# Performance work log

Measured on AMD Instinct MI355X. Metric: run time of the kernel, lower is better.

The kernel has to match this reference:

```python
import jax, jax.numpy as jnp
import numpy as np

B, S, D = 1, 2048, 1024
L, H, NH = 256, 1024, 16  # latent_dim, hidden_dim, num_heads
HD = H // NH
EPS = 1e-6


def rmsnorm(x, g):
    return x * jax.lax.rsqrt(jnp.mean(x * x, axis=-1, keepdims=True) + EPS) * g


def setup_inputs() -> dict:
    key = jax.random.key(0)
    ks = jax.random.split(key, 16)
    def w(k, shape, fan_in):
        return jax.random.normal(k, shape, jnp.float32) / np.sqrt(fan_in)
    return {
        "x": jax.random.normal(ks[0], (B, S, D), jnp.float32),
        "g1": jnp.ones((D,), jnp.float32),
        "Wq": w(ks[1], (D, H), D), "bq": jnp.zeros((H,), jnp.float32),
        "Wdown": w(ks[2], (D, L), D), "bdown": jnp.zeros((L,), jnp.float32),
        "Wk": w(ks[3], (L, H), L), "bk": jnp.zeros((H,), jnp.float32),
        "Wv": w(ks[4], (L, H), L), "bv": jnp.zeros((H,), jnp.float32),
        "Wo": w(ks[5], (H, D), H), "bo": jnp.zeros((D,), jnp.float32),
        "g2": jnp.ones((D,), jnp.float32),
        "W1": w(ks[6], (D, 4 * D), D), "b1": jnp.zeros((4 * D,), jnp.float32),
        "W2": w(ks[7], (4 * D, D), 4 * D), "b2": jnp.zeros((D,), jnp.float32),
    }


def reference(x, g1, Wq, bq, Wdown, bdown, Wk, bk, Wv, bv, Wo, bo, g2, W1, b1, W2, b2):
    stream = x
    # RMSNorm -> MLA (low-rank latent KV attention, causal)
    h = rmsnorm(x, g1)
    q = (h @ Wq + bq).reshape(B, S, NH, HD)
    c = h @ Wdown + bdown                       # [B,S,L] compressed KV latent
    k = (c @ Wk + bk).reshape(B, S, NH, HD)
    v = (c @ Wv + bv).reshape(B, S, NH, HD)
    scores = jnp.einsum("bqhd,bkhd->bhqk", q, k) / np.sqrt(HD)
    causal = jnp.tril(jnp.ones((S, S), bool))
    scores = jnp.where(causal, scores, jnp.finfo(scores.dtype).min)
    attn = jax.nn.softmax(scores, axis=-1)
    o = jnp.einsum("bhqk,bkhd->bqhd", attn, v).reshape(B, S, H)
    stream = (o @ Wo + bo) + stream
    # RMSNorm -> FFN (D -> 4D -> D, activation on every layer incl. last)
    h = rmsnorm(stream, g2)
    h = jax.nn.silu(h @ W1 + b1)
    h = jax.nn.silu(h @ W2 + b2)
    return h + stream
```

## Files before the change

### kernel.cpp

```cpp
#include <hip/hip_runtime.h>

typedef __bf16 bf16x8 __attribute__((ext_vector_type(8)));
typedef float  f32x4  __attribute__((ext_vector_type(4)));

static __device__ __forceinline__ ushort f2bf(float f) {
    union { float f; unsigned u; } a; a.f = f;
    unsigned r = a.u + 0x7FFFu + ((a.u >> 16) & 1u);
    return (ushort)(r >> 16);
}
static __device__ __forceinline__ ushort f2bf_hw(float f) {
    __bf16 b = (__bf16)f;
    return __builtin_bit_cast(ushort, b);
}

#define TS  2048
#define TD  1024
#define TL  256
#define TH  1024
#define TNH 16
#define THD 64
#define TDF 4096
#define ATT_CE 0.18033688f

#define GLD_LDS(gp, lp) \
    __builtin_amdgcn_global_load_lds( \
        (const __attribute__((address_space(1))) unsigned int*)(gp), \
        (__attribute__((address_space(3))) unsigned int*)(lp), 16, 0, 0)

__global__ __launch_bounds__(256) void transpose_to_bf16(
    const float* __restrict__ in, ushort* __restrict__ out, int K, int N)
{
    __shared__ float tile[32][33];
    const int k0 = blockIdx.x * 32, n0 = blockIdx.y * 32;
    const int tx = threadIdx.x, ty = threadIdx.y;
#pragma unroll
    for (int i = ty; i < 32; i += 8)
        tile[i][tx] = in[(size_t)(k0 + i) * N + n0 + tx];
    __syncthreads();
#pragma unroll
    for (int i = ty; i < 32; i += 8)
        out[(size_t)(n0 + i) * K + k0 + tx] = f2bf(tile[tx][i]);
}

__global__ __launch_bounds__(256) void concat_bias_kernel(
    const float* __restrict__ a, const float* __restrict__ b,
    float* __restrict__ o, int n)
{
    const int i = blockIdx.x * 256 + threadIdx.x;
    o[i] = (i < n) ? a[i] : b[i - n];
}

__global__ __launch_bounds__(256) void rmsnorm_kernel(
    const float* __restrict__ x, const float* __restrict__ g,
    ushort* __restrict__ out, int D)
{
    const int row = blockIdx.x;
    const int tid = threadIdx.x;
    const float4 v = ((const float4*)(x + (size_t)row * D))[tid];
    float ss = v.x * v.x + v.y * v.y + v.z * v.z + v.w * v.w;
#pragma unroll
    for (int off = 32; off > 0; off >>= 1) ss += __shfl_down(ss, off);
    __shared__ float sums[4];
    if ((tid & 63) == 0) sums[tid >> 6] = ss;
    __syncthreads();
    const float tot = sums[0] + sums[1] + sums[2] + sums[3];
    const float scale = rsqrtf(tot / (float)D + 1e-6f);
    const float4 gv = ((const float4*)g)[tid];
    ushort4 o;
    o.x = f2bf(v.x * scale * gv.x);
    o.y = f2bf(v.y * scale * gv.y);
    o.z = f2bf(v.z * scale * gv.z);
    o.w = f2bf(v.w * scale * gv.w);
    *(ushort4*)(out + (size_t)row * D + tid * 4) = o;
}

template <int EPI, int BM, int BN, int BKH>
__global__ __launch_bounds__(256) void gemm_bf16_kernel(
    const ushort* __restrict__ A, const ushort* __restrict__ BT,
    const float* __restrict__ bias, const float* __restrict__ resid,
    void* __restrict__ outp, int M, int N, int K)
{
    constexpr int WM = BM / 2, WN = BN / 2;
    constexpr int MT = WM / 16, NT = WN / 16;
    constexpr int NLA = BM / 64, NLB = BN / 64;
    __shared__ alignas(16) ushort As[2][BKH][BM * 32];
    __shared__ alignas(16) ushort Bs[2][BKH][BN * 32];
    const int bm = blockIdx.y * BM, bn = blockIdx.x * BN;
    const int tid = threadIdx.x;
    const int lane = tid & 63, wave = tid >> 6;
    const int wr = (wave >> 1) * WM, wc = (wave & 1) * WN;
    const int l15 = lane & 15, l4 = lane >> 4;

    f32x4 acc[MT][NT] = {};

    const int grow = wave * 16 + (lane >> 2);
    const int gcol = (lane & 3) * 8;
    const ushort* Ag = A + (size_t)(bm + grow) * K + gcol;
    const ushort* Bg = BT + (size_t)(bn + grow) * K + gcol;

    auto stage = [&](int buf, int k0) {
#pragma unroll
        for (int h = 0; h < BKH; ++h) {
#pragma unroll
            for (int i = 0; i < NLA; ++i)
                GLD_LDS(Ag + (size_t)(i * 64) * K + k0 + h * 32,
                        &As[buf][h][(i * 64 + wave * 16) * 32]);
#pragma unroll
            for (int i = 0; i < NLB; ++i)
                GLD_LDS(Bg + (size_t)(i * 64) * K + k0 + h * 32,
                        &Bs[buf][h][(i * 64 + wave * 16) * 32]);
        }
    };

    stage(0, 0);
    asm volatile("s_waitcnt vmcnt(0)" ::: "memory");
    __syncthreads();

    const int nsteps = K / (32 * BKH);
    for (int t = 0; t < nsteps; ++t) {
        const int cur = t & 1;
        if (t + 1 < nsteps) stage(cur ^ 1, (t + 1) * 32 * BKH);

#pragma unroll
        for (int h = 0; h < BKH; ++h) {
            bf16x8 af[MT], bf[NT];
#pragma unroll
            for (int mt = 0; mt < MT; ++mt)
                af[mt] = *(const bf16x8*)&As[cur][h][(wr + mt * 16 + l15) * 32 + l4 * 8];
#pragma unroll
            for (int nt = 0; nt < NT; ++nt)
                bf[nt] = *(const bf16x8*)&Bs[cur][h][(wc + nt * 16 + l15) * 32 + l4 * 8];
#pragma unroll
            for (int mt = 0; mt < MT; ++mt)
#pragma unroll
                for (int nt = 0; nt < NT; ++nt)
                    acc[mt][nt] = __builtin_amdgcn_mfma_f32_16x16x32_bf16(
                        af[mt], bf[nt], acc[mt][nt], 0, 0, 0);
        }

        asm volatile("s_waitcnt vmcnt(0)" ::: "memory");
        __syncthreads();
    }

#pragma unroll
    for (int mt = 0; mt < MT; ++mt) {
#pragma unroll
        for (int nt = 0; nt < NT; ++nt) {
#pragma unroll
            for (int i = 0; i < 4; ++i) {
                const int row = bm + wr + mt * 16 + l4 * 4 + i;
                const int col = bn + wc + nt * 16 + l15;
                float v = acc[mt][nt][i] + bias[col];
                if constexpr (EPI == 1 || EPI == 3) v = v / (1.f + __expf(-v));
                if constexpr (EPI == 2 || EPI == 3) v += resid[(size_t)row * N + col];
                if constexpr (EPI == 0 || EPI == 1)
                    ((ushort*)outp)[(size_t)row * N + col] = f2bf(v);
                else
                    ((float*)outp)[(size_t)row * N + col] = v;
            }
        }
    }
}

__global__ __launch_bounds__(256) void mla_attn_kernel(
    const ushort* __restrict__ Q, const ushort* __restrict__ Kg,
    const ushort* __restrict__ Vg, float* __restrict__ OP, float* __restrict__ ML)
{
    constexpr int QSTR = 1024, KSTR = 2048;
    __shared__ alignas(16) ushort Ks[2][64 * 64];
    __shared__ alignas(16) ushort VTs[2][64 * 64];
    __shared__ alignas(16) ushort Ps[4][16 * 64];
    const int qb = (int)gridDim.x - 1 - (int)blockIdx.x;
    const int h = blockIdx.y;
    const int sp = blockIdx.z;
    const int tid = threadIdx.x, lane = tid & 63, wave = tid >> 6;
    const int l15 = lane & 15, l4 = lane >> 4;
    const int qrow0 = qb * 64 + wave * 16;
    const int myq = qrow0 + l15;

    const int ntile = qb + 1;
    const int half = (ntile + 1) >> 1;
    const int kt0 = sp ? half : 0;
    const int ktend = sp ? ntile : half;

    auto swzK = [](ushort* base, int row, int colbyte) -> ushort* {
        return (ushort*)((char*)base + row * 128 + (colbyte ^ ((row & 7) << 4)));
    };
    auto swzVT = [](ushort* base, int d, int colbyte) -> ushort* {
        return (ushort*)((char*)base + d * 128 + (colbyte ^ (((d >> 3) & 7) << 4)));
    };
    auto swzP = [&](int row, int colbyte) -> ushort* {
        return (ushort*)((char*)&Ps[wave][0] + row * 128 + (colbyte ^ ((row & 7) << 4)));
    };

    bf16x8 qf[2];
#pragma unroll
    for (int ks = 0; ks < 2; ++ks)
        qf[ks] = *(const bf16x8*)&Q[(size_t)(qrow0 + l15) * QSTR + h * THD + ks * 32 + l4 * 8];

    f32x4 oacc[4] = {};
    float m_run = -1e30f, l_run = 0.f;

    const int sr = tid >> 3, sc = (tid & 7) * 8;
    const ushort* kbase = Kg + (size_t)sr * KSTR + h * THD + sc;
    const ushort* vbase = Vg + (size_t)sr * KSTR + h * THD + sc;

    uint4 kr0, kr1, vr0, vr1;
    {
        const size_t off = (size_t)kt0 * 64 * KSTR;
        kr0 = *(const uint4*)(kbase + off);
        kr1 = *(const uint4*)(kbase + off + (size_t)32 * KSTR);
        vr0 = *(const uint4*)(vbase + off);
        vr1 = *(const uint4*)(vbase + off + (size_t)32 * KSTR);
    }
    {
        *(uint4*)swzK(&Ks[0][0], sr, sc * 2) = kr0;
        *(uint4*)swzK(&Ks[0][0], sr + 32, sc * 2) = kr1;
        const ushort* p0 = (const ushort*)&vr0;
        const ushort* p1 = (const ushort*)&vr1;
#pragma unroll
        for (int j = 0; j < 8; ++j) {
            *swzVT(&VTs[0][0], sc + j, sr * 2) = p0[j];
            *swzVT(&VTs[0][0], sc + j, (sr + 32) * 2) = p1[j];
        }
    }
    if (kt0 + 1 < ktend) {
        const size_t off = (size_t)(kt0 + 1) * 64 * KSTR;
        kr0 = *(const uint4*)(kbase + off);
        kr1 = *(const uint4*)(kbase + off + (size_t)32 * KSTR);
        vr0 = *(const uint4*)(vbase + off);
        vr1 = *(const uint4*)(vbase + off + (size_t)32 * KSTR);
    }

    for (int kt = kt0; kt < ktend; ++kt) {
        const int rel = kt - kt0;
        __syncthreads();
        if (kt + 1 < ktend) {
            ushort* kd = &Ks[(rel + 1) & 1][0];
            ushort* vd = &VTs[(rel + 1) & 1][0];
            *(uint4*)swzK(kd, sr, sc * 2) = kr0;
            *(uint4*)swzK(kd, sr + 32, sc * 2) = kr1;
            const ushort* p0 = (const ushort*)&vr0;
            const ushort* p1 = (const ushort*)&vr1;
#pragma unroll
            for (int j = 0; j < 8; ++j) {
                *swzVT(vd, sc + j, sr * 2) = p0[j];
                *swzVT(vd, sc + j, (sr + 32) * 2) = p1[j];
            }
            if (kt + 2 < ktend) {
                const size_t off = (size_t)(kt + 2) * 64 * KSTR;
                kr0 = *(const uint4*)(kbase + off);
                kr1 = *(const uint4*)(kbase + off + (size_t)32 * KSTR);
                vr0 = *(const uint4*)(vbase + off);
                vr1 = *(const uint4*)(vbase + off + (size_t)32 * KSTR);
            }
        }
        const ushort* kb_lds = &Ks[rel & 1][0];
        const ushort* vb_lds = &VTs[rel & 1][0];

        f32x4 s[4] = {};
        __builtin_amdgcn_s_setprio(1);
#pragma unroll
        for (int ks = 0; ks < 2; ++ks) {
#pragma unroll
            for (int nt = 0; nt < 4; ++nt) {
                const bf16x8 kf = *(const bf16x8*)swzK((ushort*)kb_lds, nt * 16 + l15, ks * 64 + l4 * 16);
                s[nt] = __builtin_amdgcn_mfma_f32_16x16x32_bf16(kf, qf[ks], s[nt], 0, 0, 0);
            }
        }
        __builtin_amdgcn_s_setprio(0);

        if (kt == qb) {
            const int kb = kt * 64;
#pragma unroll
            for (int nt = 0; nt < 4; ++nt)
#pragma unroll
                for (int i = 0; i < 4; ++i)
                    if (kb + nt * 16 + l4 * 4 + i > myq) s[nt][i] = -3.0e38f;
        }

        float mx = m_run;
#pragma unroll
        for (int nt = 0; nt < 4; ++nt)
#pragma unroll
            for (int i = 0; i < 4; ++i) mx = fmaxf(mx, s[nt][i]);
        mx = fmaxf(mx, __shfl_xor(mx, 16));
        mx = fmaxf(mx, __shfl_xor(mx, 32));
        const float alpha = exp2f((m_run - mx) * ATT_CE);
        m_run = mx;
        float ps = 0.f;
#pragma unroll
        for (int nt = 0; nt < 4; ++nt)
#pragma unroll
            for (int i = 0; i < 4; ++i) {
                const float p = exp2f((s[nt][i] - mx) * ATT_CE);
                s[nt][i] = p;
                ps += p;
            }
        ps += __shfl_xor(ps, 16);
        ps += __shfl_xor(ps, 32);
        l_run = l_run * alpha + ps;

#pragma unroll
        for (int dt = 0; dt < 4; ++dt)
#pragma unroll
            for (int i = 0; i < 4; ++i) oacc[dt][i] *= alpha;

#pragma unroll
        for (int nt = 0; nt < 4; ++nt) {
            ushort4 pk;
            pk.x = f2bf_hw(s[nt][0]); pk.y = f2bf_hw(s[nt][1]);
            pk.z = f2bf_hw(s[nt][2]); pk.w = f2bf_hw(s[nt][3]);
            *(ushort4*)swzP(l15, nt * 32 + l4 * 8) = pk;
        }

        __builtin_amdgcn_s_setprio(1);
#pragma unroll
        for (int ks = 0; ks < 2; ++ks) {
            const bf16x8 pf = *(const bf16x8*)swzP(l15, ks * 64 + l4 * 16);
#pragma unroll
            for (int dt = 0; dt < 4; ++dt) {
                const bf16x8 vf = *(const bf16x8*)swzVT((ushort*)vb_lds, dt * 16 + l15, ks * 64 + l4 * 16);
                oacc[dt] = __builtin_amdgcn_mfma_f32_16x16x32_bf16(vf, pf, oacc[dt], 0, 0, 0);
            }
        }
        __builtin_amdgcn_s_setprio(0);
    }

    float* op = OP + (size_t)sp * TS * TH;
#pragma unroll
    for (int dt = 0; dt < 4; ++dt) {
        float4 o4;
        o4.x = oacc[dt][0]; o4.y = oacc[dt][1];
        o4.z = oacc[dt][2]; o4.w = oacc[dt][3];
        *(float4*)&op[(size_t)myq * TH + h * THD + dt * 16 + l4 * 4] = o4;
    }
    if (l4 == 0) {
        float* ml = ML + (size_t)sp * TS * TNH * 2;
        ml[((size_t)myq * TNH + h) * 2 + 0] = m_run;
        ml[((size_t)myq * TNH + h) * 2 + 1] = l_run;
    }
}

__global__ __launch_bounds__(256) void attn_combine_kernel(
    const float* __restrict__ OP, const float* __restrict__ ML,
    ushort* __restrict__ O)
{
    const int idx = blockIdx.x * 256 + threadIdx.x;
    const int row = idx >> 8;
    const int h = (idx & 255) >> 4;
    const float m0 = ML[((size_t)row * TNH + h) * 2 + 0];
    const float l0 = ML[((size_t)row * TNH + h) * 2 + 1];
    const float m1 = ML[(size_t)TS * TNH * 2 + ((size_t)row * TNH + h) * 2 + 0];
    const float l1 = ML[(size_t)TS * TNH * 2 + ((size_t)row * TNH + h) * 2 + 1];
    const float M = fmaxf(m0, m1);
    const float w0 = exp2f((m0 - M) * ATT_CE);
    const float w1 = exp2f((m1 - M) * ATT_CE);
    const float inv = 1.f / (l0 * w0 + l1 * w1);
    const float4 a = ((const float4*)OP)[idx];
    const float4 b = ((const float4*)(OP + (size_t)TS * TH))[idx];
    ushort4 o;
    o.x = f2bf_hw((a.x * w0 + b.x * w1) * inv);
    o.y = f2bf_hw((a.y * w0 + b.y * w1) * inv);
    o.z = f2bf_hw((a.z * w0 + b.z * w1) * inv);
    o.w = f2bf_hw((a.w * w0 + b.w * w1) * inv);
    ((ushort4*)O)[idx] = o;
}

extern "C" void kernel_launch(void* const* d_in, const int* in_sizes, int n_in,
                              void* d_out, int out_size, void* d_ws, size_t ws_size,
                              hipStream_t stream)
{
    const float* x     = (const float*)d_in[0];
    const float* g1    = (const float*)d_in[1];
    const float* Wq    = (const float*)d_in[2];
    const float* bq    = (const float*)d_in[3];
    const float* Wdown = (const float*)d_in[4];
    const float* bdown = (const float*)d_in[5];
    const float* Wk    = (const float*)d_in[6];
    const float* bk    = (const float*)d_in[7];
    const float* Wv    = (const float*)d_in[8];
    const float* bv    = (const float*)d_in[9];
    const float* Wo    = (const float*)d_in[10];
    const float* bo    = (const float*)d_in[11];
    const float* g2    = (const float*)d_in[12];
    const float* W1    = (const float*)d_in[13];
    const float* b1    = (const float*)d_in[14];
    const float* W2    = (const float*)d_in[15];
    const float* b2    = (const float*)d_in[16];
    float* out = (float*)d_out;

    char* ws = (char*)d_ws;
    size_t off = 0;
    auto alloc = [&](size_t bytes) {
        void* p = ws + off;
        off += (bytes + 255) & ~(size_t)255;
        return p;
    };
    ushort* WqT    = (ushort*)alloc((size_t)TH * TD * 2);
    ushort* WdownT = (ushort*)alloc((size_t)TL * TD * 2);
    ushort* WkvT   = (ushort*)alloc((size_t)2 * TH * TL * 2);
    ushort* WoT    = (ushort*)alloc((size_t)TD * TH * 2);
    ushort* W1T    = (ushort*)alloc((size_t)TDF * TD * 2);
    ushort* W2T    = (ushort*)alloc((size_t)TD * TDF * 2);
    float*  bkv    = (float*)alloc((size_t)2 * TH * 4);
    ushort* hbuf   = (ushort*)alloc((size_t)TS * TD * 2);
    ushort* cbuf   = (ushort*)alloc((size_t)TS * TL * 2);
    ushort* qbuf   = (ushort*)alloc((size_t)TS * TH * 2);
    ushort* kvbuf  = (ushort*)alloc((size_t)TS * 2 * TH * 2);
    ushort* obuf   = (ushort*)alloc((size_t)TS * TH * 2);
    float*  strm   = (float*)alloc((size_t)TS * TD * 4);
    ushort* h2buf  = (ushort*)alloc((size_t)TS * TD * 2);
    ushort* ffn1   = (ushort*)alloc((size_t)TS * TDF * 2);
    float*  mlbuf  = (float*)alloc((size_t)2 * TS * TNH * 2 * 4);
    float*  opart  = (float*)ffn1;

    const dim3 tb(32, 8);
    transpose_to_bf16<<<dim3(TD / 32, TH / 32), tb, 0, stream>>>(Wq, WqT, TD, TH);
    transpose_to_bf16<<<dim3(TD / 32, TL / 32), tb, 0, stream>>>(Wdown, WdownT, TD, TL);
    transpose_to_bf16<<<dim3(TL / 32, TH / 32), tb, 0, stream>>>(Wk, WkvT, TL, TH);
    transpose_to_bf16<<<dim3(TL / 32, TH / 32), tb, 0, stream>>>(Wv, WkvT + (size_t)TH * TL, TL, TH);
    transpose_to_bf16<<<dim3(TH / 32, TD / 32), tb, 0, stream>>>(Wo, WoT, TH, TD);
    transpose_to_bf16<<<dim3(TD / 32, TDF / 32), tb, 0, stream>>>(W1, W1T, TD, TDF);
    transpose_to_bf16<<<dim3(TDF / 32, TD / 32), tb, 0, stream>>>(W2, W2T, TDF, TD);
    concat_bias_kernel<<<(2 * TH) / 256, 256, 0, stream>>>(bk, bv, bkv, TH);

    rmsnorm_kernel<<<TS, 256, 0, stream>>>(x, g1, hbuf, TD);

    gemm_bf16_kernel<0, 64, 64, 2><<<dim3(TH / 64, TS / 64), 256, 0, stream>>>(
        hbuf, WqT, bq, nullptr, qbuf, TS, TH, TD);
    gemm_bf16_kernel<0, 64, 64, 2><<<dim3(TL / 64, TS / 64), 256, 0, stream>>>(
        hbuf, WdownT, bdown, nullptr, cbuf, TS, TL, TD);
    gemm_bf16_kernel<0, 64, 64, 2><<<dim3(2 * TH / 64, TS / 64), 256, 0, stream>>>(
        cbuf, WkvT, bkv, nullptr, kvbuf, TS, 2 * TH, TL);

    mla_attn_kernel<<<dim3(TS / 64, TNH, 2), 256, 0, stream>>>(
        qbuf, kvbuf, kvbuf + TH, opart, mlbuf);
    attn_combine_kernel<<<(TS * TH / 4) / 256, 256, 0, stream>>>(
        opart, mlbuf, obuf);

    gemm_bf16_kernel<2, 64, 64, 2><<<dim3(TD / 64, TS / 64), 256, 0, stream>>>(
        obuf, WoT, bo, x, strm, TS, TD, TH);

    rmsnorm_kernel<<<TS, 256, 0, stream>>>(strm, g2, h2buf, TD);

    gemm_bf16_kernel<1, 128, 128, 1><<<dim3(TDF / 128, TS / 128), 256, 0, stream>>>(
        h2buf, W1T, b1, nullptr, ffn1, TS, TDF, TD);
    gemm_bf16_kernel<3, 64, 64, 2><<<dim3(TD / 64, TS / 64), 256, 0, stream>>>(
        ffn1, W2T, b2, strm, out, TS, TD, TDF);
}
```

Before: 216.4 us.

## Process two query groups per wave, split keys four ways, store bf16 partials

The attention kernel now covers 128 query rows per block, with each wave handling two 16-row groups. Both groups share the same K and V tiles loaded into LDS, which halves K/V staging per query row. The key range is split into four chunks instead of two, so the causal workload stays spread across the same block count. Partial outputs are written as bf16 rather than fp32 to cut combine traffic, at the cost of extra rounding. Higher register pressure from doubled accumulators, now capped by a launch bound of 4, may limit occupancy.

```diff
diff --git a/kernel.cpp b/kernel.cpp
--- a/kernel.cpp
+++ b/kernel.cpp
@@ -11,6 +11,9 @@
 static __device__ __forceinline__ ushort f2bf_hw(float f) {
     __bf16 b = (__bf16)f;
     return __builtin_bit_cast(ushort, b);
+}
+static __device__ __forceinline__ float bf2f(ushort u) {
+    return __builtin_bit_cast(float, (unsigned)u << 16);
 }
 
 #define TS  2048
@@ -21,6 +24,7 @@
 #define THD 64
 #define TDF 4096
 #define ATT_CE 0.18033688f
+#define NSPLIT 4
 
 #define GLD_LDS(gp, lp) \
     __builtin_amdgcn_global_load_lds( \
@@ -162,9 +166,9 @@
     }
 }
 
-__global__ __launch_bounds__(256) void mla_attn_kernel(
+__global__ __launch_bounds__(256, 4) void mla_attn_kernel(
     const ushort* __restrict__ Q, const ushort* __restrict__ Kg,
-    const ushort* __restrict__ Vg, float* __restrict__ OP, float* __restrict__ ML)
+    const ushort* __restrict__ Vg, ushort* __restrict__ OP, float* __restrict__ ML)
 {
     constexpr int QSTR = 1024, KSTR = 2048;
     __shared__ alignas(16) ushort Ks[2][64 * 64];
@@ -175,13 +179,14 @@
     const int sp = blockIdx.z;
     const int tid = threadIdx.x, lane = tid & 63, wave = tid >> 6;
     const int l15 = lane & 15, l4 = lane >> 4;
-    const int qrow0 = qb * 64 + wave * 16;
-    const int myq = qrow0 + l15;
-
-    const int ntile = qb + 1;
-    const int half = (ntile + 1) >> 1;
-    const int kt0 = sp ? half : 0;
-    const int ktend = sp ? ntile : half;
+    const int qrow0 = qb * 128 + wave * 32;
+    const int myqA = qrow0 + l15;
+    const int myqB = qrow0 + 16 + l15;
+
+    const int ntile = 2 * (qb + 1);
+    const int chunk = (ntile + NSPLIT - 1) / NSPLIT;
+    const int kt0 = sp * chunk;
+    const int ktend = min(ntile, kt0 + chunk);
 
     auto swzK = [](ushort* base, int row, int colbyte) -> ushort* {
         return (ushort*)((char*)base + row * 128 + (colbyte ^ ((row & 7) << 4)));
@@ -193,43 +198,45 @@
         return (ushort*)((char*)&Ps[wave][0] + row * 128 + (colbyte ^ ((row & 7) << 4)));
     };
 
-    bf16x8 qf[2];
-#pragma unroll
-    for (int ks = 0; ks < 2; ++ks)
-        qf[ks] = *(const bf16x8*)&Q[(size_t)(qrow0 + l15) * QSTR + h * THD + ks * 32 + l4 * 8];
-
-    f32x4 oacc[4] = {};
-    float m_run = -1e30f, l_run = 0.f;
+    bf16x8 qfA[2], qfB[2];
+#pragma unroll
+    for (int ks = 0; ks < 2; ++ks) {
+        qfA[ks] = *(const bf16x8*)&Q[(size_t)myqA * QSTR + h * THD + ks * 32 + l4 * 8];
+        qfB[ks] = *(const bf16x8*)&Q[(size_t)myqB * QSTR + h * THD + ks * 32 + l4 * 8];
+    }
+
+    f32x4 oaccA[4] = {}, oaccB[4] = {};
+    float mA = -1e30f, lA = 0.f, mB = -1e30f, lB = 0.f;
 
     const int sr = tid >> 3, sc = (tid & 7) * 8;
     const ushort* kbase = Kg + (size_t)sr * KSTR + h * THD + sc;
     const ushort* vbase = Vg + (size_t)sr * KSTR + h * THD + sc;
 
     uint4 kr0, kr1, vr0, vr1;
-    {
-        const size_t off = (size_t)kt0 * 64 * KSTR;
-        kr0 = *(const uint4*)(kbase + off);
-        kr1 = *(const uint4*)(kbase + off + (size_t)32 * KSTR);
-        vr0 = *(const uint4*)(vbase + off);
-        vr1 = *(const uint4*)(vbase + off + (size_t)32 * KSTR);
-    }
-    {
-        *(uint4*)swzK(&Ks[0][0], sr, sc * 2) = kr0;
-        *(uint4*)swzK(&Ks[0][0], sr + 32, sc * 2) = kr1;
-        const ushort* p0 = (const ushort*)&vr0;
-        const ushort* p1 = (const ushort*)&vr1;
-#pragma unroll
-        for (int j = 0; j < 8; ++j) {
-            *swzVT(&VTs[0][0], sc + j, sr * 2) = p0[j];
-            *swzVT(&VTs[0][0], sc + j, (sr + 32) * 2) = p1[j];
-        }
-    }
-    if (kt0 + 1 < ktend) {
-        const size_t off = (size_t)(kt0 + 1) * 64 * KSTR;
-        kr0 = *(const uint4*)(kbase + off);
-        kr1 = *(const uint4*)(kbase + off + (size_t)32 * KSTR);
-        vr0 = *(const uint4*)(vbase + off);
-        vr1 = *(const uint4*)(vbase + off + (size_t)32 * KSTR);
+    if (kt0 < ktend) {
+        {
+            const size_t off = (size_t)kt0 * 64 * KSTR;
+            kr0 = *(const uint4*)(kbase + off);
+            kr1 = *(const uint4*)(kbase + off + (size_t)32 * KSTR);
+            vr0 = *(const uint4*)(vbase + off);
+            vr1 = *(const uint4*)(vbase + off + (size_t)32 * KSTR);
+            *(uint4*)swzK(&Ks[0][0], sr, sc * 2) = kr0;
+            *(uint4*)swzK(&Ks[0][0], sr + 32, sc * 2) = kr1;
+            const ushort* p0 = (const ushort*)&vr0;
+            const ushort* p1 = (const ushort*)&vr1;
+#pragma unroll
+            for (int j = 0; j < 8; ++j) {
+                *swzVT(&VTs[0][0], sc + j, sr * 2) = p0[j];
+                *swzVT(&VTs[0][0], sc + j, (sr + 32) * 2) = p1[j];
+            }
+        }
+        if (kt0 + 1 < ktend) {
+            const size_t off = (size_t)(kt0 + 1) * 64 * KSTR;
+            kr0 = *(const uint4*)(kbase + off);
+            kr1 = *(const uint4*)(kbase + off + (size_t)32 * KSTR);
+            vr0 = *(const uint4*)(vbase + off);
+            vr1 = *(const uint4*)(vbase + off + (size_t)32 * KSTR);
+        }
     }
 
     for (int kt = kt0; kt < ktend; ++kt) {
@@ -258,112 +265,180 @@
         const ushort* kb_lds = &Ks[rel & 1][0];
         const ushort* vb_lds = &VTs[rel & 1][0];
 
-        f32x4 s[4] = {};
+        f32x4 sA[4] = {}, sB[4] = {};
         __builtin_amdgcn_s_setprio(1);
 #pragma unroll
         for (int ks = 0; ks < 2; ++ks) {
 #pragma unroll
             for (int nt = 0; nt < 4; ++nt) {
                 const bf16x8 kf = *(const bf16x8*)swzK((ushort*)kb_lds, nt * 16 + l15, ks * 64 + l4 * 16);
-                s[nt] = __builtin_amdgcn_mfma_f32_16x16x32_bf16(kf, qf[ks], s[nt], 0, 0, 0);
+                sA[nt] = __builtin_amdgcn_mfma_f32_16x16x32_bf16(kf, qfA[ks], sA[nt], 0, 0, 0);
+                sB[nt] = __builtin_amdgcn_mfma_f32_16x16x32_bf16(kf, qfB[ks], sB[nt], 0, 0, 0);
             }
         }
         __builtin_amdgcn_s_setprio(0);
 
-        if (kt == qb) {
-            const int kb = kt * 64;
+        if (kt >= 2 * qb) {
 #pragma unroll
             for (int nt = 0; nt < 4; ++nt)
 #pragma unroll
-                for (int i = 0; i < 4; ++i)
-                    if (kb + nt * 16 + l4 * 4 + i > myq) s[nt][i] = -3.0e38f;
-        }
-
-        float mx = m_run;
-#pragma unroll
-        for (int nt = 0; nt < 4; ++nt)
-#pragma unroll
-            for (int i = 0; i < 4; ++i) mx = fmaxf(mx, s[nt][i]);
-        mx = fmaxf(mx, __shfl_xor(mx, 16));
-        mx = fmaxf(mx, __shfl_xor(mx, 32));
-        const float alpha = exp2f((m_run - mx) * ATT_CE);
-        m_run = mx;
-        float ps = 0.f;
-#pragma unroll
-        for (int nt = 0; nt < 4; ++nt)
-#pragma unroll
-            for (int i = 0; i < 4; ++i) {
-                const float p = exp2f((s[nt][i] - mx) * ATT_CE);
-                s[nt][i] = p;
-                ps += p;
-            }
-        ps += __shfl_xor(ps, 16);
-        ps += __shfl_xor(ps, 32);
-        l_run = l_run * alpha + ps;
-
-#pragma unroll
-        for (int dt = 0; dt < 4; ++dt)
-#pragma unroll
-            for (int i = 0; i < 4; ++i) oacc[dt][i] *= alpha;
-
-#pragma unroll
-        for (int nt = 0; nt < 4; ++nt) {
-            ushort4 pk;
-            pk.x = f2bf_hw(s[nt][0]); pk.y = f2bf_hw(s[nt][1]);
-            pk.z = f2bf_hw(s[nt][2]); pk.w = f2bf_hw(s[nt][3]);
-            *(ushort4*)swzP(l15, nt * 32 + l4 * 8) = pk;
-        }
-
-        __builtin_amdgcn_s_setprio(1);
-#pragma unroll
-        for (int ks = 0; ks < 2; ++ks) {
-            const bf16x8 pf = *(const bf16x8*)swzP(l15, ks * 64 + l4 * 16);
-#pragma unroll
-            for (int dt = 0; dt < 4; ++dt) {
-                const bf16x8 vf = *(const bf16x8*)swzVT((ushort*)vb_lds, dt * 16 + l15, ks * 64 + l4 * 16);
-                oacc[dt] = __builtin_amdgcn_mfma_f32_16x16x32_bf16(vf, pf, oacc[dt], 0, 0, 0);
-            }
-        }
-        __builtin_amdgcn_s_setprio(0);
-    }
-
-    float* op = OP + (size_t)sp * TS * TH;
+                for (int i = 0; i < 4; ++i) {
+                    const int key = kt * 64 + nt * 16 + l4 * 4 + i;
+                    if (key > myqA) sA[nt][i] = -3.0e38f;
+                    if (key > myqB) sB[nt][i] = -3.0e38f;
+                }
+        }
+
+        {
+            float mx = mA;
+#pragma unroll
+            for (int nt = 0; nt < 4; ++nt)
+#pragma unroll
+                for (int i = 0; i < 4; ++i) mx = fmaxf(mx, sA[nt][i]);
+            mx = fmaxf(mx, __shfl_xor(mx, 16));
+            mx = fmaxf(mx, __shfl_xor(mx, 32));
+            const float alpha = exp2f((mA - mx) * ATT_CE);
+            mA = mx;
+            float ps = 0.f;
+#pragma unroll
+            for (int nt = 0; nt < 4; ++nt)
+#pragma unroll
+                for (int i = 0; i < 4; ++i) {
+                    const float p = exp2f((sA[nt][i] - mx) * ATT_CE);
+                    sA[nt][i] = p;
+                    ps += p;
+                }
+            ps += __shfl_xor(ps, 16);
+            ps += __shfl_xor(ps, 32);
+            lA = lA * alpha + ps;
+#pragma unroll
+            for (int dt = 0; dt < 4; ++dt)
+#pragma unroll
+                for (int i = 0; i < 4; ++i) oaccA[dt][i] *= alpha;
+#pragma unroll
+            for (int nt = 0; nt < 4; ++nt) {
+                ushort4 pk;
+                pk.x = f2bf_hw(sA[nt][0]); pk.y = f2bf_hw(sA[nt][1]);
+                pk.z = f2bf_hw(sA[nt][2]); pk.w = f2bf_hw(sA[nt][3]);
+                *(ushort4*)swzP(l15, nt * 32 + l4 * 8) = pk;
+            }
+            __builtin_amdgcn_s_setprio(1);
+#pragma unroll
+            for (int ks = 0; ks < 2; ++ks) {
+                const bf16x8 pf = *(const bf16x8*)swzP(l15, ks * 64 + l4 * 16);
+#pragma unroll
+                for (int dt = 0; dt < 4; ++dt) {
+                    const bf16x8 vf = *(const bf16x8*)swzVT((ushort*)vb_lds, dt * 16 + l15, ks * 64 + l4 * 16);
+                    oaccA[dt] = __builtin_amdgcn_mfma_f32_16x16x32_bf16(vf, pf, oaccA[dt], 0, 0, 0);
+                }
+            }
+            __builtin_amdgcn_s_setprio(0);
+        }
+
+        {
+            float mx = mB;
+#pragma unroll
+            for (int nt = 0; nt < 4; ++nt)
+#pragma unroll
+                for (int i = 0; i < 4; ++i) mx = fmaxf(mx, sB[nt][i]);
+            mx = fmaxf(mx, __shfl_xor(mx, 16));
+            mx = fmaxf(mx, __shfl_xor(mx, 32));
+            const float alpha = exp2f((mB - mx) * ATT_CE);
+            mB = mx;
+            float ps = 0.f;
+#pragma unroll
+            for (int nt = 0; nt < 4; ++nt)
+#pragma unroll
+                for (int i = 0; i < 4; ++i) {
+                    const float p = exp2f((sB[nt][i] - mx) * ATT_CE);
+                    sB[nt][i] = p;
+                    ps += p;
+                }
+            ps += __shfl_xor(ps, 16);
+            ps += __shfl_xor(ps, 32);
+            lB = lB * alpha + ps;
+#pragma unroll
+            for (int dt = 0; dt < 4; ++dt)
+#pragma unroll
+                for (int i = 0; i < 4; ++i) oaccB[dt][i] *= alpha;
+#pragma unroll
+            for (int nt = 0; nt < 4; ++nt) {
+                ushort4 pk;
+                pk.x = f2bf_hw(sB[nt][0]); pk.y = f2bf_hw(sB[nt][1]);
+                pk.z = f2bf_hw(sB[nt][2]); pk.w = f2bf_hw(sB[nt][3]);
+                *(ushort4*)swzP(l15, nt * 32 + l4 * 8) = pk;
+            }
+            __builtin_amdgcn_s_setprio(1);
+#pragma unroll
+            for (int ks = 0; ks < 2; ++ks) {
+                const bf16x8 pf = *(const bf16x8*)swzP(l15, ks * 64 + l4 * 16);
+#pragma unroll
+                for (int dt = 0; dt < 4; ++dt) {
+                    const bf16x8 vf = *(const bf16x8*)swzVT((ushort*)vb_lds, dt * 16 + l15, ks * 64 + l4 * 16);
+                    oaccB[dt] = __builtin_amdgcn_mfma_f32_16x16x32_bf16(vf, pf, oaccB[dt], 0, 0, 0);
+                }
+            }
+            __builtin_amdgcn_s_setprio(0);
+        }
+    }
+
+    ushort* op = OP + (size_t)sp * TS * TH;
 #pragma unroll
     for (int dt = 0; dt < 4; ++dt) {
-        float4 o4;
-        o4.x = oacc[dt][0]; o4.y = oacc[dt][1];
-        o4.z = oacc[dt][2]; o4.w = oacc[dt][3];
-        *(float4*)&op[(size_t)myq * TH + h * THD + dt * 16 + l4 * 4] = o4;
+        ushort4 a4, b4;
+        a4.x = f2bf_hw(oaccA[dt][0]); a4.y = f2bf_hw(oaccA[dt][1]);
+        a4.z = f2bf_hw(oaccA[dt][2]); a4.w = f2bf_hw(oaccA[dt][3]);
+        b4.x = f2bf_hw(oaccB[dt][0]); b4.y = f2bf_hw(oaccB[dt][1]);
+        b4.z = f2bf_hw(oaccB[dt][2]); b4.w = f2bf_hw(oaccB[dt][3]);
+        *(ushort4*)&op[(size_t)myqA * TH + h * THD + dt * 16 + l4 * 4] = a4;
+        *(ushort4*)&op[(size_t)myqB * TH + h * THD + dt * 16 + l4 * 4] = b4;
     }
     if (l4 == 0) {
         float* ml = ML + (size_t)sp * TS * TNH * 2;
-        ml[((size_t)myq * TNH + h) * 2 + 0] = m_run;
-        ml[((size_t)myq * TNH + h) * 2 + 1] = l_run;
+        ml[((size_t)myqA * TNH + h) * 2 + 0] = mA;
+        ml[((size_t)myqA * TNH + h) * 2 + 1] = lA;
+        ml[((size_t)myqB * TNH + h) * 2 + 0] = mB;
+        ml[((size_t)myqB * TNH + h) * 2 + 1] = lB;
     }
 }
 
 __global__ __launch_bounds__(256) void attn_combine_kernel(
-    const float* __restrict__ OP, const float* __restrict__ ML,
+    const ushort* __restrict__ OP, const float* __restrict__ ML,
     ushort* __restrict__ O)
 {
     const int idx = blockIdx.x * 256 + threadIdx.x;
     const int row = idx >> 8;
     const int h = (idx & 255) >> 4;
-    const float m0 = ML[((size_t)row * TNH + h) * 2 + 0];
-    const float l0 = ML[((size_t)row * TNH + h) * 2 + 1];
-    const float m1 = ML[(size_t)TS * TNH * 2 + ((size_t)row * TNH + h) * 2 + 0];
-    const float l1 = ML[(size_t)TS * TNH * 2 + ((size_t)row * TNH + h) * 2 + 1];
-    const float M = fmaxf(m0, m1);
-    const float w0 = exp2f((m0 - M) * ATT_CE);
-    const float w1 = exp2f((m1 - M) * ATT_CE);
-    const float inv = 1.f / (l0 * w0 + l1 * w1);
-    const float4 a = ((const float4*)OP)[idx];
-    const float4 b = ((const float4*)(OP + (size_t)TS * TH))[idx];
+    float m[NSPLIT], l[NSPLIT];
+#pragma unroll
+    for (int sp = 0; sp < NSPLIT; ++sp) {
+        m[sp] = ML[((size_t)sp * TS * TNH + (size_t)row * TNH + h) * 2 + 0];
+        l[sp] = ML[((size_t)sp * TS * TNH + (size_t)row * TNH + h) * 2 + 1];
+    }
+    float M = m[0];
+#pragma unroll
+    for (int sp = 1; sp < NSPLIT; ++sp) M = fmaxf(M, m[sp]);
+    float w[NSPLIT], den = 0.f;
+#pragma unroll
+    for (int sp = 0; sp < NSPLIT; ++sp) {
+        w[sp] = exp2f((m[sp] - M) * ATT_CE);
+        den += l[sp] * w[sp];
+    }
+    const float inv = 1.f / den;
+    float ax = 0.f, ay = 0.f, az = 0.f, aw = 0.f;
+#pragma unroll
+    for (int sp = 0; sp < NSPLIT; ++sp) {
+        const ushort4 u = ((const ushort4*)(OP + (size_t)sp * TS * TH))[idx];
+        ax += w[sp] * bf2f(u.x);
+        ay += w[sp] * bf2f(u.y);
+        az += w[sp] * bf2f(u.z);
+        aw += w[sp] * bf2f(u.w);
+    }
     ushort4 o;
-    o.x = f2bf_hw((a.x * w0 + b.x * w1) * inv);
-    o.y = f2bf_hw((a.y * w0 + b.y * w1) * inv);
-    o.z = f2bf_hw((a.z * w0 + b.z * w1) * inv);
-    o.w = f2bf_hw((a.w * w0 + b.w * w1) * inv);
+    o.x = f2bf_hw(ax * inv);
+    o.y = f2bf_hw(ay * inv);
+    o.z = f2bf_hw(az * inv);
+    o.w = f2bf_hw(aw * inv);
     ((ushort4*)O)[idx] = o;
 }
 
@@ -412,8 +487,8 @@
     float*  strm   = (float*)alloc((size_t)TS * TD * 4);
     ushort* h2buf  = (ushort*)alloc((size_t)TS * TD * 2);
     ushort* ffn1   = (ushort*)alloc((size_t)TS * TDF * 2);
-    float*  mlbuf  = (float*)alloc((size_t)2 * TS * TNH * 2 * 4);
-    float*  opart  = (float*)ffn1;
+    float*  mlbuf  = (float*)alloc((size_t)NSPLIT * TS * TNH * 2 * 4);
+    ushort* opart  = (ushort*)ffn1;
 
     const dim3 tb(32, 8);
     transpose_to_bf16<<<dim3(TD / 32, TH / 32), tb, 0, stream>>>(Wq, WqT, TD, TH);
@@ -434,7 +509,7 @@
     gemm_bf16_kernel<0, 64, 64, 2><<<dim3(2 * TH / 64, TS / 64), 256, 0, stream>>>(
         cbuf, WkvT, bkv, nullptr, kvbuf, TS, 2 * TH, TL);
 
-    mla_attn_kernel<<<dim3(TS / 64, TNH, 2), 256, 0, stream>>>(
+    mla_attn_kernel<<<dim3(TS / 128, TNH, NSPLIT), 256, 0, stream>>>(
         qbuf, kvbuf, kvbuf + TH, opart, mlbuf);
     attn_combine_kernel<<<(TS * TH / 4) / 256, 256, 0, stream>>>(
         opart, mlbuf, obuf);
```

Result: slower. 243.9 us (+12.7%).
